# Kernel tuning notes

Measured on AMD Instinct MI355X. Metric: run time of the kernel, lower is better.

Reference implementation:

```python
import jax, jax.numpy as jnp
import numpy as np

B, J, L = 32, 16, 4096
MU_P = 0.15
MASK_ID = 103
VOCAB = 30522


def setup_inputs() -> dict:
    key = jax.random.key(0)
    k1, k2, k3 = jax.random.split(key, 3)
    input_ids = jax.random.randint(k1, (B, J, L), 0, VOCAB, dtype=jnp.int64 if jax.config.jax_enable_x64 else jnp.int32)
    # first half: nonnegative per-token weights; second half: shared-token ids (unused by the math)
    my_attention_mask = jax.random.uniform(k2, (B, J, 2 * L), dtype=jnp.float32)
    # uniform noise for Gumbel keys (weighted sampling w/o replacement)
    u = jax.random.uniform(k3, (B, J, L), dtype=jnp.float32, minval=1e-6, maxval=1.0)
    return {"input_ids": input_ids, "my_attention_mask": my_attention_mask, "u": u}


def reference(input_ids, my_attention_mask, u):
    # Split the mask: first half holds sampling weights (second half is unused).
    Lh = my_attention_mask.shape[-1] // 2
    w = my_attention_mask[..., :Lh]                       # [B, J, L]
    nz = w > 0                                            # valid positions
    cnt = nz.sum(axis=-1)                                 # [B, J] number of nonzero weights
    num_to_mask = jnp.floor(MU_P * cnt.astype(w.dtype)).astype(jnp.int32)  # int(mu_p * len)

    # Gumbel-key trick == weighted permutation without replacement over nonzero positions.
    g = -jnp.log(-jnp.log(u))
    scores = jnp.where(nz, jnp.log(jnp.maximum(w, 1e-30)) + g, -jnp.inf)
    # rank of each position in descending-score order
    rank = jnp.argsort(jnp.argsort(-scores, axis=-1), axis=-1)
    sel = (rank < num_to_mask[..., None]) & nz            # [B, J, L] positions to mask

    out_mask = sel.astype(w.dtype)
    out_ids = jnp.where(sel, jnp.asarray(MASK_ID, dtype=input_ids.dtype), input_ids)
    return out_ids, out_mask, -out_mask
```

## Files before the change

kernel.cpp:

```cpp
#include <hip/hip_runtime.h>

#define L_LEN 4096
#define NT 512
#define EPT (L_LEN / NT)
#define V4I (L_LEN / (NT * 4))
#define EQ_CAP 128
#define ROWS 512

__global__ __launch_bounds__(NT) void AttentionEssentialReinforce_51238959841470_kernel(
    const int* __restrict__ ids,
    const float* __restrict__ amask,
    const float* __restrict__ uin,
    float* __restrict__ out,
    int n_per)
{
    __shared__ unsigned long long keys[L_LEN];
    __shared__ unsigned int hist[256];
    __shared__ int eqlist[EQ_CAP];
    __shared__ unsigned int s_cnt, s_eqn, s_remk, s_csel, s_or;
    __shared__ unsigned long long s_prefix;

    const int row = blockIdx.x;
    const int tid = threadIdx.x;
    const float* wrow = amask + (size_t)row * (2 * L_LEN);
    const float* urow = uin + (size_t)row * L_LEN;

    if (tid == 0) { s_cnt = 0; s_eqn = 0; s_or = 0; }
    __syncthreads();

    if (((const unsigned*)ids)[2 * tid + 1] != 0u) s_or = 1u;

    unsigned localnz = 0;
    #pragma unroll
    for (int it = 0; it < V4I; ++it) {
        int v4 = it * NT + tid;
        float4 wv = reinterpret_cast<const float4*>(wrow)[v4];
        float4 uv = reinterpret_cast<const float4*>(urow)[v4];
        float wa[4] = {wv.x, wv.y, wv.z, wv.w};
        float ua[4] = {uv.x, uv.y, uv.z, uv.w};
        #pragma unroll
        for (int m = 0; m < 4; ++m) {
            unsigned long long kk = 0ULL;
            if (wa[m] > 0.0f) {
                double t = -log((double)ua[m]);
                double r = (double)fmaxf(wa[m], 1e-30f) / t;
                kk = (unsigned long long)__double_as_longlong(r);
                localnz++;
            }
            keys[v4 * 4 + m] = kk;
        }
    }
    unsigned v = localnz;
    #pragma unroll
    for (int off = 32; off > 0; off >>= 1) v += __shfl_down(v, off, 64);
    if ((tid & 63) == 0) atomicAdd(&s_cnt, v);
    __syncthreads();

    const bool is64 = (s_or == 0u);
    const int cnt = (int)s_cnt;
    const int k = (int)floorf(0.15f * (float)cnt);

    unsigned long long T = ~0ULL;
    bool tie = false;
    unsigned eq_take = 0, n_eq = 0;

    if (k > 0) {
        unsigned remk = (unsigned)k, csel = 0;
        unsigned long long prefix = 0;
        int p;
        for (p = 7; p >= 0; --p) {
            if (tid < 256) hist[tid] = 0;
            __syncthreads();
            #pragma unroll
            for (int s = 0; s < EPT; ++s) {
                unsigned long long kk = keys[s * NT + tid];
                if (p == 7 || (kk >> ((p + 1) * 8)) == prefix)
                    atomicAdd(&hist[(unsigned)((kk >> (p * 8)) & 0xFFULL)], 1u);
            }
            __syncthreads();
            if (tid < 64) {
                unsigned c[4], lsum = 0;
                #pragma unroll
                for (int m = 0; m < 4; ++m) { c[m] = hist[255 - 4 * tid - m]; lsum += c[m]; }
                unsigned scan = lsum;
                #pragma unroll
                for (int off = 1; off < 64; off <<= 1) {
                    unsigned o = __shfl_up(scan, (unsigned)off, 64);
                    if (tid >= off) scan += o;
                }
                unsigned run = scan - lsum;
                #pragma unroll
                for (int m = 0; m < 4; ++m) {
                    if (run < remk && run + c[m] >= remk) {
                        s_prefix = (prefix << 8) | (unsigned long long)(255 - 4 * tid - m);
                        s_remk = remk - run;
                        s_csel = c[m];
                    }
                    run += c[m];
                }
            }
            __syncthreads();
            prefix = s_prefix; remk = s_remk; csel = s_csel;
            if (remk == csel) break;
        }
        if (p >= 0) {
            T = prefix << (p * 8);
        } else {
            tie = true;
            T = prefix;
            eq_take = remk;
            #pragma unroll
            for (int s = 0; s < EPT; ++s) {
                int i = s * NT + tid;
                if (keys[i] == T) {
                    unsigned pos = atomicAdd(&s_eqn, 1u);
                    if (pos < EQ_CAP) eqlist[pos] = i;
                }
            }
            __syncthreads();
            n_eq = s_eqn; if (n_eq > EQ_CAP) n_eq = EQ_CAP;
        }
    }

    const size_t obase = (size_t)row * L_LEN;
    float* o0 = out + obase;
    float* o1 = out + (size_t)n_per + obase;
    float* o2 = out + 2 * (size_t)n_per + obase;
    const int* idrow32 = ids + (size_t)row * L_LEN;
    const long long* idrow64 = (const long long*)ids + (size_t)row * L_LEN;

    #pragma unroll
    for (int it = 0; it < V4I; ++it) {
        int v4 = it * NT + tid;
        int ida[4];
        if (!is64) {
            int4 t = reinterpret_cast<const int4*>(idrow32)[v4];
            ida[0] = t.x; ida[1] = t.y; ida[2] = t.z; ida[3] = t.w;
        } else {
            longlong2 a = reinterpret_cast<const longlong2*>(idrow64)[2 * v4];
            longlong2 b = reinterpret_cast<const longlong2*>(idrow64)[2 * v4 + 1];
            ida[0] = (int)a.x; ida[1] = (int)a.y; ida[2] = (int)b.x; ida[3] = (int)b.y;
        }
        float f0[4], f1[4], f2[4];
        #pragma unroll
        for (int m = 0; m < 4; ++m) {
            int i = v4 * 4 + m;
            unsigned long long kk = keys[i];
            bool sel;
            if (!tie) {
                sel = (kk >= T);
            } else {
                sel = (kk > T);
                if (kk == T) {
                    int rnk = 0;
                    for (unsigned e = 0; e < n_eq; ++e) rnk += (eqlist[e] < i);
                    sel = (rnk < (int)eq_take);
                }
            }
            f0[m] = sel ? 103.0f : (float)ida[m];
            f1[m] = sel ? 1.0f : 0.0f;
            f2[m] = sel ? -1.0f : -0.0f;
        }
        reinterpret_cast<float4*>(o0)[v4] = make_float4(f0[0], f0[1], f0[2], f0[3]);
        reinterpret_cast<float4*>(o1)[v4] = make_float4(f1[0], f1[1], f1[2], f1[3]);
        reinterpret_cast<float4*>(o2)[v4] = make_float4(f2[0], f2[1], f2[2], f2[3]);
    }
}

extern "C" void kernel_launch(void* const* d_in, const int* in_sizes, int n_in,
                              void* d_out, int out_size, void* d_ws, size_t ws_size,
                              hipStream_t stream) {
    const int*   ids   = (const int*)d_in[0];
    const float* amask = (const float*)d_in[1];
    const float* uin   = (const float*)d_in[2];
    float* out = (float*)d_out;

    const int n_per = ROWS * L_LEN;

    AttentionEssentialReinforce_51238959841470_kernel<<<dim3(ROWS), dim3(NT), 0, stream>>>(
        ids, amask, uin, out, n_per);
}
```

Before: 95.53 us.

## Keep radix-select keys in registers with 1024 threads and a wider first digit

Each row block now uses 1024 threads, each holding its four 64-bit keys in registers, so the 32 KB shared key array is gone along with its store and reload traffic. The radix select switches from eight 8-bit passes to a 12-bit first digit, then 8-bit digits, then a final 4-bit digit. This can cut the number of histogram passes, because the top 12 bits of positive doubles carry sign and exponent. The 4096-bin histogram needs a block-wide two-level scan with extra barriers, and the larger block may limit occupancy.

```diff
diff --git a/kernel.cpp b/kernel.cpp
--- a/kernel.cpp
+++ b/kernel.cpp
@@ -1,11 +1,9 @@
 #include <hip/hip_runtime.h>
 
 #define L_LEN 4096
-#define NT 512
-#define EPT (L_LEN / NT)
-#define V4I (L_LEN / (NT * 4))
+#define NT 1024
+#define ROWS 512
 #define EQ_CAP 128
-#define ROWS 512
 
 __global__ __launch_bounds__(NT) void AttentionEssentialReinforce_51238959841470_kernel(
     const int* __restrict__ ids,
@@ -14,14 +12,15 @@
     float* __restrict__ out,
     int n_per)
 {
-    __shared__ unsigned long long keys[L_LEN];
-    __shared__ unsigned int hist[256];
+    __shared__ unsigned int hist[4096];
+    __shared__ unsigned int s_wtot[16], s_woff[16];
     __shared__ int eqlist[EQ_CAP];
     __shared__ unsigned int s_cnt, s_eqn, s_remk, s_csel, s_or;
     __shared__ unsigned long long s_prefix;
 
     const int row = blockIdx.x;
     const int tid = threadIdx.x;
+    const int lane = tid & 63, wid = tid >> 6;
     const float* wrow = amask + (size_t)row * (2 * L_LEN);
     const float* urow = uin + (size_t)row * L_LEN;
 
@@ -30,30 +29,27 @@
 
     if (((const unsigned*)ids)[2 * tid + 1] != 0u) s_or = 1u;
 
+    float4 wv = reinterpret_cast<const float4*>(wrow)[tid];
+    float4 uv = reinterpret_cast<const float4*>(urow)[tid];
+    float wa[4] = {wv.x, wv.y, wv.z, wv.w};
+    float ua[4] = {uv.x, uv.y, uv.z, uv.w};
+    unsigned long long kk[4];
     unsigned localnz = 0;
     #pragma unroll
-    for (int it = 0; it < V4I; ++it) {
-        int v4 = it * NT + tid;
-        float4 wv = reinterpret_cast<const float4*>(wrow)[v4];
-        float4 uv = reinterpret_cast<const float4*>(urow)[v4];
-        float wa[4] = {wv.x, wv.y, wv.z, wv.w};
-        float ua[4] = {uv.x, uv.y, uv.z, uv.w};
-        #pragma unroll
-        for (int m = 0; m < 4; ++m) {
-            unsigned long long kk = 0ULL;
-            if (wa[m] > 0.0f) {
-                double t = -log((double)ua[m]);
-                double r = (double)fmaxf(wa[m], 1e-30f) / t;
-                kk = (unsigned long long)__double_as_longlong(r);
-                localnz++;
-            }
-            keys[v4 * 4 + m] = kk;
-        }
+    for (int m = 0; m < 4; ++m) {
+        unsigned long long key = 0ULL;
+        if (wa[m] > 0.0f) {
+            double t = -log((double)ua[m]);
+            double r = (double)fmaxf(wa[m], 1e-30f) / t;
+            key = (unsigned long long)__double_as_longlong(r);
+            localnz++;
+        }
+        kk[m] = key;
     }
     unsigned v = localnz;
     #pragma unroll
     for (int off = 32; off > 0; off >>= 1) v += __shfl_down(v, off, 64);
-    if ((tid & 63) == 0) atomicAdd(&s_cnt, v);
+    if (lane == 0) atomicAdd(&s_cnt, v);
     __syncthreads();
 
     const bool is64 = (s_or == 0u);
@@ -65,56 +61,104 @@
     unsigned eq_take = 0, n_eq = 0;
 
     if (k > 0) {
+        const int SH[8] = {52, 44, 36, 28, 20, 12, 4, 0};
+        const int WD[8] = {12,  8,  8,  8,  8,  8, 8, 4};
         unsigned remk = (unsigned)k, csel = 0;
         unsigned long long prefix = 0;
-        int p;
-        for (p = 7; p >= 0; --p) {
-            if (tid < 256) hist[tid] = 0;
+        int pi;
+        for (pi = 0; pi < 8; ++pi) {
+            const int shift = SH[pi], width = WD[pi];
+            const int nb = 1 << width, sw = shift + width;
+            for (int b = tid; b < nb; b += NT) hist[b] = 0;
             __syncthreads();
             #pragma unroll
-            for (int s = 0; s < EPT; ++s) {
-                unsigned long long kk = keys[s * NT + tid];
-                if (p == 7 || (kk >> ((p + 1) * 8)) == prefix)
-                    atomicAdd(&hist[(unsigned)((kk >> (p * 8)) & 0xFFULL)], 1u);
-            }
-            __syncthreads();
-            if (tid < 64) {
+            for (int m = 0; m < 4; ++m) {
+                unsigned long long key = kk[m];
+                bool match = (sw >= 64) || ((key >> sw) == prefix);
+                if (match)
+                    atomicAdd(&hist[(unsigned)((key >> shift) & (unsigned)(nb - 1))], 1u);
+            }
+            __syncthreads();
+            if (width == 12) {
+                int b0 = 4095 - 4 * tid;
                 unsigned c[4], lsum = 0;
                 #pragma unroll
-                for (int m = 0; m < 4; ++m) { c[m] = hist[255 - 4 * tid - m]; lsum += c[m]; }
+                for (int m = 0; m < 4; ++m) { c[m] = hist[b0 - m]; lsum += c[m]; }
                 unsigned scan = lsum;
                 #pragma unroll
                 for (int off = 1; off < 64; off <<= 1) {
                     unsigned o = __shfl_up(scan, (unsigned)off, 64);
-                    if (tid >= off) scan += o;
-                }
-                unsigned run = scan - lsum;
+                    if (lane >= off) scan += o;
+                }
+                if (lane == 63) s_wtot[wid] = scan;
+                __syncthreads();
+                if (tid < 16) {
+                    unsigned acc = 0;
+                    for (int w2 = 0; w2 < tid; ++w2) acc += s_wtot[w2];
+                    s_woff[tid] = acc;
+                }
+                __syncthreads();
+                unsigned run = s_woff[wid] + (scan - lsum);
                 #pragma unroll
                 for (int m = 0; m < 4; ++m) {
                     if (run < remk && run + c[m] >= remk) {
-                        s_prefix = (prefix << 8) | (unsigned long long)(255 - 4 * tid - m);
+                        s_prefix = (prefix << 12) | (unsigned long long)(b0 - m);
                         s_remk = remk - run;
                         s_csel = c[m];
                     }
                     run += c[m];
                 }
+            } else if (width == 8) {
+                if (tid < 64) {
+                    unsigned c[4], lsum = 0;
+                    #pragma unroll
+                    for (int m = 0; m < 4; ++m) { c[m] = hist[255 - 4 * tid - m]; lsum += c[m]; }
+                    unsigned scan = lsum;
+                    #pragma unroll
+                    for (int off = 1; off < 64; off <<= 1) {
+                        unsigned o = __shfl_up(scan, (unsigned)off, 64);
+                        if (tid >= off) scan += o;
+                    }
+                    unsigned run = scan - lsum;
+                    #pragma unroll
+                    for (int m = 0; m < 4; ++m) {
+                        if (run < remk && run + c[m] >= remk) {
+                            s_prefix = (prefix << 8) | (unsigned long long)(255 - 4 * tid - m);
+                            s_remk = remk - run;
+                            s_csel = c[m];
+                        }
+                        run += c[m];
+                    }
+                }
+            } else {
+                if (tid == 0) {
+                    unsigned run = 0;
+                    for (int b = 15; b >= 0; --b) {
+                        unsigned c = hist[b];
+                        if (run < remk && run + c >= remk) {
+                            s_prefix = (prefix << 4) | (unsigned long long)b;
+                            s_remk = remk - run;
+                            s_csel = c;
+                        }
+                        run += c;
+                    }
+                }
             }
             __syncthreads();
             prefix = s_prefix; remk = s_remk; csel = s_csel;
             if (remk == csel) break;
         }
-        if (p >= 0) {
-            T = prefix << (p * 8);
+        if (pi < 8) {
+            T = prefix << SH[pi];
         } else {
             tie = true;
             T = prefix;
             eq_take = remk;
             #pragma unroll
-            for (int s = 0; s < EPT; ++s) {
-                int i = s * NT + tid;
-                if (keys[i] == T) {
+            for (int m = 0; m < 4; ++m) {
+                if (kk[m] == T) {
                     unsigned pos = atomicAdd(&s_eqn, 1u);
-                    if (pos < EQ_CAP) eqlist[pos] = i;
+                    if (pos < EQ_CAP) eqlist[pos] = 4 * tid + m;
                 }
             }
             __syncthreads();
@@ -126,45 +170,38 @@
     float* o0 = out + obase;
     float* o1 = out + (size_t)n_per + obase;
     float* o2 = out + 2 * (size_t)n_per + obase;
-    const int* idrow32 = ids + (size_t)row * L_LEN;
-    const long long* idrow64 = (const long long*)ids + (size_t)row * L_LEN;
-
+
+    int ida[4];
+    if (!is64) {
+        int4 t4 = reinterpret_cast<const int4*>(ids + (size_t)row * L_LEN)[tid];
+        ida[0] = t4.x; ida[1] = t4.y; ida[2] = t4.z; ida[3] = t4.w;
+    } else {
+        const longlong2* idr = reinterpret_cast<const longlong2*>(
+            (const long long*)ids + (size_t)row * L_LEN);
+        longlong2 a = idr[2 * tid], b = idr[2 * tid + 1];
+        ida[0] = (int)a.x; ida[1] = (int)a.y; ida[2] = (int)b.x; ida[3] = (int)b.y;
+    }
+    float f0[4], f1[4], f2[4];
     #pragma unroll
-    for (int it = 0; it < V4I; ++it) {
-        int v4 = it * NT + tid;
-        int ida[4];
-        if (!is64) {
-            int4 t = reinterpret_cast<const int4*>(idrow32)[v4];
-            ida[0] = t.x; ida[1] = t.y; ida[2] = t.z; ida[3] = t.w;
+    for (int m = 0; m < 4; ++m) {
+        bool sel;
+        if (!tie) {
+            sel = (kk[m] >= T);
         } else {
-            longlong2 a = reinterpret_cast<const longlong2*>(idrow64)[2 * v4];
-            longlong2 b = reinterpret_cast<const longlong2*>(idrow64)[2 * v4 + 1];
-            ida[0] = (int)a.x; ida[1] = (int)a.y; ida[2] = (int)b.x; ida[3] = (int)b.y;
-        }
-        float f0[4], f1[4], f2[4];
-        #pragma unroll
-        for (int m = 0; m < 4; ++m) {
-            int i = v4 * 4 + m;
-            unsigned long long kk = keys[i];
-            bool sel;
-            if (!tie) {
-                sel = (kk >= T);
-            } else {
-                sel = (kk > T);
-                if (kk == T) {
-                    int rnk = 0;
-                    for (unsigned e = 0; e < n_eq; ++e) rnk += (eqlist[e] < i);
-                    sel = (rnk < (int)eq_take);
-                }
-            }
-            f0[m] = sel ? 103.0f : (float)ida[m];
-            f1[m] = sel ? 1.0f : 0.0f;
-            f2[m] = sel ? -1.0f : -0.0f;
-        }
-        reinterpret_cast<float4*>(o0)[v4] = make_float4(f0[0], f0[1], f0[2], f0[3]);
-        reinterpret_cast<float4*>(o1)[v4] = make_float4(f1[0], f1[1], f1[2], f1[3]);
-        reinterpret_cast<float4*>(o2)[v4] = make_float4(f2[0], f2[1], f2[2], f2[3]);
-    }
+            sel = (kk[m] > T);
+            if (kk[m] == T) {
+                int i = 4 * tid + m, rnk = 0;
+                for (unsigned e = 0; e < n_eq; ++e) rnk += (eqlist[e] < i);
+                sel = (rnk < (int)eq_take);
+            }
+        }
+        f0[m] = sel ? 103.0f : (float)ida[m];
+        f1[m] = sel ? 1.0f : 0.0f;
+        f2[m] = sel ? -1.0f : -0.0f;
+    }
+    reinterpret_cast<float4*>(o0)[tid] = make_float4(f0[0], f0[1], f0[2], f0[3]);
+    reinterpret_cast<float4*>(o1)[tid] = make_float4(f1[0], f1[1], f1[2], f1[3]);
+    reinterpret_cast<float4*>(o2)[tid] = make_float4(f2[0], f2[1], f2[2], f2[3]);
 }
 
 extern "C" void kernel_launch(void* const* d_in, const int* in_sizes, int n_in,
```

Result: no change. 94.31 us (-1.3%).

## Replace 8-pass double radix select with single fp32 12-bit histogram plus exact boundary refinement

Applied to the files above, without the earlier changes.

Keys are now computed in fp32 as 32-bit values, and a 4096-bin histogram on the top 12 bits is built during key generation. One scan finds the bin containing the k-th key. Only elements within a small slop window around that bin are recomputed in double precision and ranked exactly against a boundary buffer. The block shrinks to a single 64-thread wavefront, which removes most block-wide barriers and the multi-pass radix loops. The cost is less parallelism per row, a fixed-capacity boundary buffer (BCAP), and a reliance on SLOP being wide enough to cover fp32-vs-double rounding differences.

```diff
diff --git a/kernel.cpp b/kernel.cpp
--- a/kernel.cpp
+++ b/kernel.cpp
@@ -1,11 +1,11 @@
 #include <hip/hip_runtime.h>
 
 #define L_LEN 4096
-#define NT 512
-#define EPT (L_LEN / NT)
-#define V4I (L_LEN / (NT * 4))
-#define EQ_CAP 128
+#define NT 64
+#define CHUNKS 16
 #define ROWS 512
+#define SLOP 48u
+#define BCAP 512
 
 __global__ __launch_bounds__(NT) void AttentionEssentialReinforce_51238959841470_kernel(
     const int* __restrict__ ids,
@@ -14,113 +14,119 @@
     float* __restrict__ out,
     int n_per)
 {
-    __shared__ unsigned long long keys[L_LEN];
-    __shared__ unsigned int hist[256];
-    __shared__ int eqlist[EQ_CAP];
-    __shared__ unsigned int s_cnt, s_eqn, s_remk, s_csel, s_or;
-    __shared__ unsigned long long s_prefix;
+    __shared__ unsigned int keys[L_LEN];
+    __shared__ unsigned int hist[4096];
+    __shared__ unsigned long long bkey[BCAP];
+    __shared__ int bidx[BCAP];
+    __shared__ unsigned int s_prefix, s_remk, s_bn;
 
     const int row = blockIdx.x;
-    const int tid = threadIdx.x;
+    const int lane = threadIdx.x;
     const float* wrow = amask + (size_t)row * (2 * L_LEN);
     const float* urow = uin + (size_t)row * L_LEN;
 
-    if (tid == 0) { s_cnt = 0; s_eqn = 0; s_or = 0; }
+    const bool is64 = (__ballot(((const unsigned*)ids)[2 * lane + 1] != 0u) == 0ULL);
+
+    if (lane == 0) s_bn = 0;
+    {
+        uint4 z = make_uint4(0, 0, 0, 0);
+        for (int j = 0; j < 16; ++j)
+            reinterpret_cast<uint4*>(hist)[j * NT + lane] = z;
+    }
     __syncthreads();
 
-    if (((const unsigned*)ids)[2 * tid + 1] != 0u) s_or = 1u;
-
-    unsigned localnz = 0;
-    #pragma unroll
-    for (int it = 0; it < V4I; ++it) {
-        int v4 = it * NT + tid;
-        float4 wv = reinterpret_cast<const float4*>(wrow)[v4];
-        float4 uv = reinterpret_cast<const float4*>(urow)[v4];
-        float wa[4] = {wv.x, wv.y, wv.z, wv.w};
-        float ua[4] = {uv.x, uv.y, uv.z, uv.w};
+    unsigned nz = 0;
+    for (int s = 0; s < CHUNKS; ++s) {
+        int v4 = s * NT + lane;
+        float4 w4 = reinterpret_cast<const float4*>(wrow)[v4];
+        float4 u4 = reinterpret_cast<const float4*>(urow)[v4];
+        float wa[4] = {w4.x, w4.y, w4.z, w4.w};
+        float ua[4] = {u4.x, u4.y, u4.z, u4.w};
+        unsigned kk[4];
         #pragma unroll
         for (int m = 0; m < 4; ++m) {
-            unsigned long long kk = 0ULL;
+            kk[m] = 0u;
             if (wa[m] > 0.0f) {
-                double t = -log((double)ua[m]);
-                double r = (double)fmaxf(wa[m], 1e-30f) / t;
-                kk = (unsigned long long)__double_as_longlong(r);
-                localnz++;
+                float t = -logf(ua[m]);
+                float r = fmaxf(wa[m], 1e-30f) / t;
+                kk[m] = __float_as_uint(r);
+                nz++;
+                atomicAdd(&hist[kk[m] >> 20], 1u);
             }
-            keys[v4 * 4 + m] = kk;
+        }
+        reinterpret_cast<uint4*>(keys)[v4] = make_uint4(kk[0], kk[1], kk[2], kk[3]);
+    }
+    #pragma unroll
+    for (int off = 32; off > 0; off >>= 1) nz += __shfl_down(nz, off, 64);
+    const int cnt = (int)__shfl(nz, 0, 64);
+    const int k = (int)floorf(0.15f * (float)cnt);
+    __syncthreads();
+
+    unsigned lsum = 0;
+    for (int j = 0; j < 16; ++j) {
+        int jj = (j + lane) & 15;
+        uint4 h = reinterpret_cast<const uint4*>(hist)[lane * 16 + jj];
+        lsum += h.x + h.y + h.z + h.w;
+    }
+    unsigned scan = lsum;
+    #pragma unroll
+    for (int off = 1; off < 64; off <<= 1) {
+        unsigned o = __shfl_up(scan, (unsigned)off, 64);
+        if (lane >= off) scan += o;
+    }
+    const unsigned total = __shfl(scan, 63, 64);
+    const unsigned higher = total - scan;
+
+    if (k > 0) {
+        unsigned remk = (unsigned)k;
+        if (higher < remk && higher + lsum >= remk) {
+            unsigned run = higher;
+            for (int b = lane * 64 + 63; b >= lane * 64; --b) {
+                unsigned c = hist[b];
+                if (run < remk && run + c >= remk) { s_prefix = (unsigned)b; s_remk = remk - run; }
+                run += c;
+            }
         }
     }
-    unsigned v = localnz;
-    #pragma unroll
-    for (int off = 32; off > 0; off >>= 1) v += __shfl_down(v, off, 64);
-    if ((tid & 63) == 0) atomicAdd(&s_cnt, v);
     __syncthreads();
 
-    const bool is64 = (s_or == 0u);
-    const int cnt = (int)s_cnt;
-    const int k = (int)floorf(0.15f * (float)cnt);
-
-    unsigned long long T = ~0ULL;
-    bool tie = false;
-    unsigned eq_take = 0, n_eq = 0;
+    unsigned lo_thr = 0xFFFFFFFFu, hi_thr = 0xFFFFFFFFu;
+    int need = 0;
+    unsigned bn = 0;
 
     if (k > 0) {
-        unsigned remk = (unsigned)k, csel = 0;
-        unsigned long long prefix = 0;
-        int p;
-        for (p = 7; p >= 0; --p) {
-            if (tid < 256) hist[tid] = 0;
-            __syncthreads();
+        const unsigned T12 = s_prefix;
+        const unsigned B_lo = T12 << 20, B_hi = (T12 << 20) | 0xFFFFFu;
+        lo_thr = (B_lo > SLOP) ? B_lo - SLOP : 1u;
+        hi_thr = B_hi + SLOP;
+
+        unsigned nhi = 0;
+        for (int s = 0; s < CHUNKS; ++s) {
+            int v4 = s * NT + lane;
+            uint4 k4 = reinterpret_cast<const uint4*>(keys)[v4];
+            unsigned ka[4] = {k4.x, k4.y, k4.z, k4.w};
             #pragma unroll
-            for (int s = 0; s < EPT; ++s) {
-                unsigned long long kk = keys[s * NT + tid];
-                if (p == 7 || (kk >> ((p + 1) * 8)) == prefix)
-                    atomicAdd(&hist[(unsigned)((kk >> (p * 8)) & 0xFFULL)], 1u);
-            }
-            __syncthreads();
-            if (tid < 64) {
-                unsigned c[4], lsum = 0;
-                #pragma unroll
-                for (int m = 0; m < 4; ++m) { c[m] = hist[255 - 4 * tid - m]; lsum += c[m]; }
-                unsigned scan = lsum;
-                #pragma unroll
-                for (int off = 1; off < 64; off <<= 1) {
-                    unsigned o = __shfl_up(scan, (unsigned)off, 64);
-                    if (tid >= off) scan += o;
-                }
-                unsigned run = scan - lsum;
-                #pragma unroll
-                for (int m = 0; m < 4; ++m) {
-                    if (run < remk && run + c[m] >= remk) {
-                        s_prefix = (prefix << 8) | (unsigned long long)(255 - 4 * tid - m);
-                        s_remk = remk - run;
-                        s_csel = c[m];
+            for (int m = 0; m < 4; ++m) {
+                if (ka[m] > hi_thr) {
+                    nhi++;
+                } else if (ka[m] >= lo_thr) {
+                    unsigned pos = atomicAdd(&s_bn, 1u);
+                    if (pos < BCAP) {
+                        int i = 4 * v4 + m;
+                        double t = -log((double)urow[i]);
+                        double r = (double)fmaxf(wrow[i], 1e-30f) / t;
+                        bkey[pos] = (unsigned long long)__double_as_longlong(r);
+                        bidx[pos] = i;
                     }
-                    run += c[m];
                 }
             }
-            __syncthreads();
-            prefix = s_prefix; remk = s_remk; csel = s_csel;
-            if (remk == csel) break;
         }
-        if (p >= 0) {
-            T = prefix << (p * 8);
-        } else {
-            tie = true;
-            T = prefix;
-            eq_take = remk;
-            #pragma unroll
-            for (int s = 0; s < EPT; ++s) {
-                int i = s * NT + tid;
-                if (keys[i] == T) {
-                    unsigned pos = atomicAdd(&s_eqn, 1u);
-                    if (pos < EQ_CAP) eqlist[pos] = i;
-                }
-            }
-            __syncthreads();
-            n_eq = s_eqn; if (n_eq > EQ_CAP) n_eq = EQ_CAP;
-        }
+        #pragma unroll
+        for (int off = 32; off > 0; off >>= 1) nhi += __shfl_down(nhi, off, 64);
+        need = k - (int)__shfl(nhi, 0, 64);
     }
+    __syncthreads();
+    if (k > 0) { bn = s_bn; if (bn > BCAP) bn = BCAP; }
 
     const size_t obase = (size_t)row * L_LEN;
     float* o0 = out + obase;
@@ -129,13 +135,14 @@
     const int* idrow32 = ids + (size_t)row * L_LEN;
     const long long* idrow64 = (const long long*)ids + (size_t)row * L_LEN;
 
-    #pragma unroll
-    for (int it = 0; it < V4I; ++it) {
-        int v4 = it * NT + tid;
+    for (int s = 0; s < CHUNKS; ++s) {
+        int v4 = s * NT + lane;
+        uint4 k4 = reinterpret_cast<const uint4*>(keys)[v4];
+        unsigned ka[4] = {k4.x, k4.y, k4.z, k4.w};
         int ida[4];
         if (!is64) {
-            int4 t = reinterpret_cast<const int4*>(idrow32)[v4];
-            ida[0] = t.x; ida[1] = t.y; ida[2] = t.z; ida[3] = t.w;
+            int4 t4 = reinterpret_cast<const int4*>(idrow32)[v4];
+            ida[0] = t4.x; ida[1] = t4.y; ida[2] = t4.z; ida[3] = t4.w;
         } else {
             longlong2 a = reinterpret_cast<const longlong2*>(idrow64)[2 * v4];
             longlong2 b = reinterpret_cast<const longlong2*>(idrow64)[2 * v4 + 1];
@@ -144,18 +151,20 @@
         float f0[4], f1[4], f2[4];
         #pragma unroll
         for (int m = 0; m < 4; ++m) {
-            int i = v4 * 4 + m;
-            unsigned long long kk = keys[i];
             bool sel;
-            if (!tie) {
-                sel = (kk >= T);
+            if (ka[m] > hi_thr) {
+                sel = true;
+            } else if (ka[m] < lo_thr) {
+                sel = false;
             } else {
-                sel = (kk > T);
-                if (kk == T) {
-                    int rnk = 0;
-                    for (unsigned e = 0; e < n_eq; ++e) rnk += (eqlist[e] < i);
-                    sel = (rnk < (int)eq_take);
-                }
+                int i = 4 * v4 + m;
+                double t = -log((double)urow[i]);
+                double r = (double)fmaxf(wrow[i], 1e-30f) / t;
+                unsigned long long myk = (unsigned long long)__double_as_longlong(r);
+                int rnk = 0;
+                for (unsigned j = 0; j < bn; ++j)
+                    rnk += (bkey[j] > myk) || (bkey[j] == myk && bidx[j] < i);
+                sel = (rnk < need);
             }
             f0[m] = sel ? 103.0f : (float)ida[m];
             f1[m] = sel ? 1.0f : 0.0f;
```

Result: slower. 332.9 us (+248.4%).
